# Kernel optimization log

Hardware: AMD Instinct MI355X
Metric: run time of the kernel (lower is better)

The kernel has to match this reference:

```python
import jax, jax.numpy as jnp
import numpy as np

SDF_W = 7000.0
EIK_W = 600.0
ORI_W = 500.0
NEAR_ORI_W = 10.0
GRADN_W = 200.0
K_NEIGHBORS = 2


def _orientation_sign(query, surface, normals, k=K_NEIGHBORS):
    # Original detaches to numpy for a scipy KDTree query -> stop_gradient here.
    q = jax.lax.stop_gradient(query)       # [Q,3]
    s = jax.lax.stop_gradient(surface)     # [S,3]
    n = jax.lax.stop_gradient(normals)     # [S,3]
    # Brute-force squared distances [Q,S] (GEMM-dominated).
    d2 = (jnp.sum(q * q, axis=-1, keepdims=True)
          - 2.0 * (q @ s.T)
          + jnp.sum(s * s, axis=-1)[None, :])
    _, idx = jax.lax.top_k(-d2, k)         # [Q,k] nearest-neighbor indices
    near_pts = s[idx]                      # [Q,k,3]
    near_nrm = n[idx]                      # [Q,k,3]
    vecs = q[:, None, :] - near_pts        # [Q,k,3]
    dots = jnp.sum(vecs * near_nrm, axis=-1)  # [Q,k]
    return jnp.sign(jnp.mean(dots, axis=1))   # [Q]


def setup_inputs() -> dict:
    key = jax.random.key(0)
    ks = jax.random.split(key, 8)
    N = 16384
    return {
        "manifold_pred": jax.random.normal(ks[0], (N, 1), jnp.float32) * 0.1,
        "manifold_grad": jax.random.normal(ks[1], (N, 3), jnp.float32),
        "nonmanifold_pred": jax.random.normal(ks[2], (N, 1), jnp.float32),
        "near_points_pred": jax.random.normal(ks[3], (N, 1), jnp.float32) * 0.1,
        "surface_points": jax.random.normal(ks[4], (N, 3), jnp.float32),
        "surface_normals": jax.random.normal(ks[5], (N, 3), jnp.float32),
        "off_surface_points": jax.random.normal(ks[6], (N, 3), jnp.float32) * 1.5,
        "near_points": jax.random.normal(ks[7], (N, 3), jnp.float32),
    }


def reference(manifold_pred, manifold_grad, nonmanifold_pred, near_points_pred,
              surface_points, surface_normals, off_surface_points, near_points):
    sdf_loss = jnp.mean(manifold_pred ** 2)
    eikonal_loss = jnp.mean((jnp.linalg.norm(manifold_grad, axis=-1) - 1.0) ** 2)

    signs_off = _orientation_sign(off_surface_points, surface_points, surface_normals)
    orientation_loss = jnp.mean(jax.nn.relu(-nonmanifold_pred * signs_off[:, None]))

    signs_near = _orientation_sign(near_points, surface_points, surface_normals)
    near_surface_orientation_loss = jnp.mean(jax.nn.relu(-near_points_pred * signs_near[:, None]))

    gradient_normal_loss = jnp.mean((manifold_grad - surface_normals) ** 2)

    total = (SDF_W * sdf_loss + EIK_W * eikonal_loss + ORI_W * orientation_loss
             + NEAR_ORI_W * near_surface_orientation_loss + GRADN_W * gradient_normal_loss)
    return (total, sdf_loss, eikonal_loss, orientation_loss,
            near_surface_orientation_loss, gradient_normal_loss)
```

## Files before the change

kernel.cpp:

```cpp
#include <hip/hip_runtime.h>
#include <math.h>

#define SDF_W      7000.0f
#define EIK_W      600.0f
#define ORI_W      500.0f
#define NEAR_ORI_W 10.0f
#define GRADN_W    200.0f

#define NWAVE  8
#define QW     16
#define CHKI   32
#define QPW    8


__device__ __forceinline__ float neg_half_norm2(float sx, float sy, float sz) {
    return -0.5f * fmaf(sx, sx, fmaf(sy, sy, sz * sz));
}
__device__ __forceinline__ float score(float qx, float qy, float qz,
                                       float sx, float sy, float sz, float nh) {
    return fmaf(qx, sx, fmaf(qy, sy, fmaf(qz, sz, nh)));
}

__device__ __forceinline__ float dot_fmt(const float4* __restrict__ fmt,
                                         const float* __restrict__ norms, int j,
                                         float qx, float qy, float qz) {
    float4 s = fmt[j];
    return fmaf(qx - s.x, norms[3*j],
           fmaf(qy - s.y, norms[3*j+1], (qz - s.z) * norms[3*j+2]));
}

__global__ __launch_bounds__(256) void fmt_k(
    const float* __restrict__ surf, float4* __restrict__ fmt, int S, int SPfull)
{
    int p = blockIdx.x * 256 + threadIdx.x;
    if (p >= SPfull) return;
    if (p < S) {
        float sx = surf[3*p], sy = surf[3*p+1], sz = surf[3*p+2];
        fmt[p] = make_float4(sx, sy, sz, neg_half_norm2(sx, sy, sz));
    } else {
        fmt[p] = make_float4(0.f, 0.f, 0.f, -3.0e38f);
    }
}

__global__ __launch_bounds__(512) __attribute__((amdgpu_waves_per_eu(2, 2)))
void nn_scan(const float* __restrict__ offq, const float* __restrict__ nearq,
             const float4* __restrict__ fmt, float4* __restrict__ recs,
             int nIter, int Qoff, int QT)
{
    const int lane = threadIdx.x & 63;
    const int wv   = __builtin_amdgcn_readfirstlane((int)threadIdx.x >> 6);
    const int qbase = (blockIdx.x * NWAVE + wv) * QW;

    float qx[QW], qy[QW], qz[QW];
    #pragma unroll
    for (int j = 0; j < QW; ++j) {
        int q = qbase + j;
        float x = 0.f, y = 0.f, z = 0.f;
        if (q < QT) {
            const float* p = (q < Qoff) ? (offq + 3 * q) : (nearq + 3 * (q - Qoff));
            x = p[0]; y = p[1]; z = p[2];
        }
        qx[j] = x; qy[j] = y; qz[j] = z;
    }

    float M1[QW], M2[QW];
    int id1[QW], id2[QW];
    #pragma unroll
    for (int j = 0; j < QW; ++j) {
        M1[j] = -3.0e38f; M2[j] = -3.0e38f; id1[j] = 0; id2[j] = 0;
    }

    const int nCh = (nIter + CHKI - 1) / CHKI;
    const float4* fp = fmt + lane;
    float4 cur = fp[0];
    int i = 0;
    #pragma unroll 1
    for (int cc = 0; cc < nCh; ++cc) {
        float P1[QW], P2[QW];
        #pragma unroll
        for (int j = 0; j < QW; ++j) { P1[j] = M1[j]; P2[j] = M2[j]; }
        const int iEnd = min(nIter, (cc + 1) * CHKI);
        #pragma unroll 2
        for (; i < iEnd; ++i) {
            float4 nxt = fp[(i + 1) * 64];
            #pragma unroll
            for (int j = 0; j < QW; ++j) {
                float g = score(qx[j], qy[j], qz[j], cur.x, cur.y, cur.z, cur.w);
                M2[j] = __builtin_amdgcn_fmed3f(g, M1[j], M2[j]);
                M1[j] = fmaxf(M1[j], g);
            }
            cur = nxt;
        }
        const int cid = (cc << 6) | lane;
        #pragma unroll
        for (int j = 0; j < QW; ++j) {
            id1[j] = (M1[j] != P1[j]) ? cid : id1[j];
            id2[j] = (M2[j] != P2[j]) ? cid : id2[j];
        }
    }

    #pragma unroll 1
    for (int j = 0; j < QW; ++j) {
        float m1 = M1[j], m2 = M2[j];
        int i1 = id1[j], i2 = id2[j];
        #pragma unroll
        for (int off = 32; off > 0; off >>= 1) {
            float b1 = __shfl_down(m1, off);
            float b2 = __shfl_down(m2, off);
            int   c1 = __shfl_down(i1, off);
            int   c2 = __shfl_down(i2, off);
            if (b1 > m1) {
                bool ka = (m1 > b2);
                m2 = ka ? m1 : b2;  i2 = ka ? i1 : c2;
                m1 = b1;            i1 = c1;
            } else {
                bool kb = (b1 > m2);
                m2 = kb ? b1 : m2;  i2 = kb ? c1 : i2;
            }
        }
        if (lane == 0 && qbase + j < QT)
            recs[qbase + j] = make_float4(m1, m2, __int_as_float(i1), __int_as_float(i2));
    }
}

__global__ __launch_bounds__(512) __attribute__((amdgpu_waves_per_eu(4, 4)))
void recover_k(const float* __restrict__ offq, const float* __restrict__ nearq,
               const float4* __restrict__ fmt, const float* __restrict__ norms,
               const float* __restrict__ nmpred, const float* __restrict__ nppred,
               const float* __restrict__ mp, const float* __restrict__ mg,
               const float* __restrict__ sn,
               const float4* __restrict__ recs, float* __restrict__ partials,
               int S, int Qoff, int QT, int N, int RB)
{
    const int t    = threadIdx.x;
    const int lane = t & 63;
    const int wv   = t >> 6;
    const int q0   = (blockIdx.x * NWAVE + wv) * QPW;

    float accOri = 0.f, accNori = 0.f;
    for (int u = 0; u < QPW; ++u) {
        int q = q0 + u;
        if (q >= QT) break;
        float4 r = recs[q];
        float M1 = r.x, M2 = r.y;
        int i1 = __float_as_int(r.z), i2 = __float_as_int(r.w);
        int cc1 = i1 >> 6, ln1 = i1 & 63;
        int cc2 = i2 >> 6, ln2 = i2 & 63;

        bool isNear = (q >= Qoff);
        const float* qp = isNear ? (nearq + 3 * (q - Qoff)) : (offq + 3 * q);
        float qx = qp[0], qy = qp[1], qz = qp[2];

        int half = lane >> 5;
        int k    = lane & 31;
        int p    = ((half ? cc2 : cc1) * CHKI + k) * 64 + (half ? ln2 : ln1);
        float target = half ? M2 : M1;
        float g = -3.0e38f, dotv = 0.f;
        if (p < S) {
            float4 s4 = fmt[p];
            g = score(qx, qy, qz, s4.x, s4.y, s4.z, s4.w);
            float nx = norms[3*p], ny = norms[3*p+1], nz = norms[3*p+2];
            dotv = fmaf(qx - s4.x, nx, fmaf(qy - s4.y, ny, (qz - s4.z) * nz));
        }
        unsigned long long m = __ballot(g == target);
        unsigned int lo = (unsigned int)m;
        unsigned int hi = (unsigned int)(m >> 32);

        float d1, d2;
        int k1 = -1;
        if (lo) {
            k1 = __ffs(lo) - 1;
            d1 = __shfl(dotv, k1);
        } else {
            d1 = dot_fmt(fmt, norms, 0, qx, qy, qz);
        }
        if (M1 == M2 && i1 == i2 && k1 >= 0) hi &= ~(1u << k1);
        if (hi) {
            int k2 = __ffs(hi) - 1;
            d2 = __shfl(dotv, 32 + k2);
        } else {
            int I1 = (k1 >= 0) ? ((cc1 * CHKI + k1) * 64 + ln1) : 0;
            int I2 = (I1 == 0 && S > 1) ? 1 : 0;
            d2 = dot_fmt(fmt, norms, I2, qx, qy, qz);
        }

        float ms = d1 + d2;
        float sgn = (ms > 0.f) ? 1.f : ((ms < 0.f) ? -1.f : 0.f);
        float pred = isNear ? nppred[q - Qoff] : nmpred[q];
        float term = fmaxf(0.f, -pred * sgn);
        if (lane == 0) {
            if (isNear) accNori += term; else accOri += term;
        }
    }

    float sdf = 0.f, eik = 0.f, gn = 0.f;
    for (int i = blockIdx.x * 512 + t; i < N; i += (int)gridDim.x * 512) {
        float p = mp[i];
        sdf += p * p;
        float gx = mg[3*i], gy = mg[3*i+1], gz = mg[3*i+2];
        float nrm = sqrtf(fmaf(gx, gx, fmaf(gy, gy, gz * gz)));
        float d = nrm - 1.0f;
        eik += d * d;
        float nx = sn[3*i], ny = sn[3*i+1], nz = sn[3*i+2];
        float dx = gx - nx, dy = gy - ny, dz = gz - nz;
        gn += fmaf(dx, dx, fmaf(dy, dy, dz * dz));
    }

    float v0 = accOri, v1 = accNori, v2 = sdf, v3 = eik, v4 = gn;
    #pragma unroll
    for (int off = 32; off > 0; off >>= 1) {
        v0 += __shfl_down(v0, off);
        v1 += __shfl_down(v1, off);
        v2 += __shfl_down(v2, off);
        v3 += __shfl_down(v3, off);
        v4 += __shfl_down(v4, off);
    }
    __shared__ float red[5][NWAVE];
    if (lane == 0) {
        red[0][wv] = v0; red[1][wv] = v1; red[2][wv] = v2;
        red[3][wv] = v3; red[4][wv] = v4;
    }
    __syncthreads();
    if (t == 0) {
        #pragma unroll
        for (int kk = 0; kk < 5; ++kk) {
            float s = 0.f;
            #pragma unroll
            for (int w = 0; w < NWAVE; ++w) s += red[kk][w];
            partials[kk * RB + blockIdx.x] = s;
        }
    }
}

__global__ __launch_bounds__(256) void final_k(
    const float* __restrict__ partials, float* __restrict__ out,
    int N, int RB, int Qoff, int Qnear)
{
    __shared__ float r[5][256];
    int t = threadIdx.x;
    float s[5] = {0.f, 0.f, 0.f, 0.f, 0.f};
    for (int i = t; i < RB; i += 256) {
        #pragma unroll
        for (int k = 0; k < 5; ++k) s[k] += partials[k * RB + i];
    }
    #pragma unroll
    for (int k = 0; k < 5; ++k) r[k][t] = s[k];
    __syncthreads();
    for (int off = 128; off > 0; off >>= 1) {
        if (t < off) {
            #pragma unroll
            for (int k = 0; k < 5; ++k) r[k][t] += r[k][t + off];
        }
        __syncthreads();
    }
    if (t == 0) {
        float orim  = r[0][0] / (float)Qoff;
        float norim = r[1][0] / (float)Qnear;
        float sdfm  = r[2][0] / (float)N;
        float eikm  = r[3][0] / (float)N;
        float gnm   = r[4][0] / (3.0f * (float)N);
        out[0] = SDF_W * sdfm + EIK_W * eikm + ORI_W * orim
               + NEAR_ORI_W * norim + GRADN_W * gnm;
        out[1] = sdfm;
        out[2] = eikm;
        out[3] = orim;
        out[4] = norim;
        out[5] = gnm;
    }
}

extern "C" void kernel_launch(void* const* d_in, const int* in_sizes, int n_in,
                              void* d_out, int out_size, void* d_ws, size_t ws_size,
                              hipStream_t stream)
{
    const float* mp    = (const float*)d_in[0];
    const float* mg    = (const float*)d_in[1];
    const float* nmp   = (const float*)d_in[2];
    const float* npp   = (const float*)d_in[3];
    const float* sp    = (const float*)d_in[4];
    const float* sn    = (const float*)d_in[5];
    const float* offp  = (const float*)d_in[6];
    const float* nearp = (const float*)d_in[7];
    float* out = (float*)d_out;

    const int N     = in_sizes[0];
    const int S     = in_sizes[4] / 3;
    const int Qoff  = in_sizes[2];
    const int Qnear = in_sizes[3];
    const int QT    = Qoff + Qnear;

    const int nIter  = (S + 63) / 64;
    const int SPfull = nIter * 64 + 64;

    float4* fmt      = (float4*)d_ws;
    float4* recs     = fmt + SPfull;
    float*  partials = (float*)(recs + QT);

    const int RB         = (QT + NWAVE * QPW - 1) / (NWAVE * QPW);
    const int scanBlocks = (QT + NWAVE * QW - 1) / (NWAVE * QW);

    fmt_k<<<(SPfull + 255) / 256, 256, 0, stream>>>(sp, fmt, S, SPfull);
    nn_scan<<<scanBlocks, 512, 0, stream>>>(offp, nearp, fmt, recs, nIter, Qoff, QT);
    recover_k<<<RB, 512, 0, stream>>>(offp, nearp, fmt, sn, nmp, npp,
                                      mp, mg, sn, recs, partials,
                                      S, Qoff, QT, N, RB);
    final_k<<<1, 256, 0, stream>>>(partials, out, N, RB, Qoff, Qnear);
}
```

Measured before the change: 179.0 us.

## Split the nearest-neighbor surface scan across two blocks and merge top-2 in recovery

The brute-force nearest-neighbor scan now divides the surface-point range into two chunk-aligned halves, each handled by a separate block. Each half writes its own top-2 record per query, and the recovery kernel merges the two partial top-2 lists before re-scoring. This doubles the number of scan blocks, which is meant to fill the GPU more fully and shorten the serial per-wave loop. The cost is an extra record write and merge per query, and the recovery kernel's occupancy hint is changed as well.

```diff
diff --git a/kernel.cpp b/kernel.cpp
--- a/kernel.cpp
+++ b/kernel.cpp
@@ -10,6 +10,7 @@
 #define NWAVE  8
 #define QW     16
 #define CHKI   32
+#define NSPLIT 2
 #define QPW    8
 
 
@@ -42,14 +43,19 @@
     }
 }
 
-__global__ __launch_bounds__(512) __attribute__((amdgpu_waves_per_eu(2, 2)))
+__global__ __launch_bounds__(512) __attribute__((amdgpu_waves_per_eu(2, 4)))
 void nn_scan(const float* __restrict__ offq, const float* __restrict__ nearq,
              const float4* __restrict__ fmt, float4* __restrict__ recs,
-             int nIter, int Qoff, int QT)
+             int nIter, int iPart, int Qoff, int QT)
 {
     const int lane = threadIdx.x & 63;
     const int wv   = __builtin_amdgcn_readfirstlane((int)threadIdx.x >> 6);
-    const int qbase = (blockIdx.x * NWAVE + wv) * QW;
+    const int part = blockIdx.x & (NSPLIT - 1);
+    const int qbase = ((blockIdx.x >> 1) * NWAVE + wv) * QW;
+
+    int iBeg = part * iPart;        if (iBeg > nIter) iBeg = nIter;
+    int iEndAll = iBeg + iPart;     if (iEndAll > nIter) iEndAll = nIter;
+    const int chunkBase = iBeg / CHKI;
 
     float qx[QW], qy[QW], qz[QW];
     #pragma unroll
@@ -70,16 +76,16 @@
         M1[j] = -3.0e38f; M2[j] = -3.0e38f; id1[j] = 0; id2[j] = 0;
     }
 
-    const int nCh = (nIter + CHKI - 1) / CHKI;
+    const int nCh = (iEndAll - iBeg + CHKI - 1) / CHKI;
     const float4* fp = fmt + lane;
-    float4 cur = fp[0];
-    int i = 0;
+    float4 cur = fp[iBeg * 64];
+    int i = iBeg;
     #pragma unroll 1
     for (int cc = 0; cc < nCh; ++cc) {
         float P1[QW], P2[QW];
         #pragma unroll
         for (int j = 0; j < QW; ++j) { P1[j] = M1[j]; P2[j] = M2[j]; }
-        const int iEnd = min(nIter, (cc + 1) * CHKI);
+        const int iEnd = min(iEndAll, iBeg + (cc + 1) * CHKI);
         #pragma unroll 2
         for (; i < iEnd; ++i) {
             float4 nxt = fp[(i + 1) * 64];
@@ -91,7 +97,7 @@
             }
             cur = nxt;
         }
-        const int cid = (cc << 6) | lane;
+        const int cid = ((chunkBase + cc) << 6) | lane;
         #pragma unroll
         for (int j = 0; j < QW; ++j) {
             id1[j] = (M1[j] != P1[j]) ? cid : id1[j];
@@ -119,11 +125,12 @@
             }
         }
         if (lane == 0 && qbase + j < QT)
-            recs[qbase + j] = make_float4(m1, m2, __int_as_float(i1), __int_as_float(i2));
-    }
-}
-
-__global__ __launch_bounds__(512) __attribute__((amdgpu_waves_per_eu(4, 4)))
+            recs[(qbase + j) * NSPLIT + part] =
+                make_float4(m1, m2, __int_as_float(i1), __int_as_float(i2));
+    }
+}
+
+__global__ __launch_bounds__(512) __attribute__((amdgpu_waves_per_eu(2, 2)))
 void recover_k(const float* __restrict__ offq, const float* __restrict__ nearq,
                const float4* __restrict__ fmt, const float* __restrict__ norms,
                const float* __restrict__ nmpred, const float* __restrict__ nppred,
@@ -141,9 +148,18 @@
     for (int u = 0; u < QPW; ++u) {
         int q = q0 + u;
         if (q >= QT) break;
-        float4 r = recs[q];
-        float M1 = r.x, M2 = r.y;
-        int i1 = __float_as_int(r.z), i2 = __float_as_int(r.w);
+
+        float M1 = -3.0e38f, M2 = -3.0e38f;
+        int i1 = 0, i2 = 0;
+        #pragma unroll
+        for (int h = 0; h < NSPLIT; ++h) {
+            float4 r = recs[q * NSPLIT + h];
+            float a1 = r.x, a2 = r.y;
+            int ac1 = __float_as_int(r.z), ac2 = __float_as_int(r.w);
+            if (a1 > M1)      { M2 = M1; i2 = i1; M1 = a1; i1 = ac1; }
+            else if (a1 > M2) { M2 = a1; i2 = ac1; }
+            if (a2 > M2)      { M2 = a2; i2 = ac2; }
+        }
         int cc1 = i1 >> 6, ln1 = i1 & 63;
         int cc2 = i2 >> 6, ln2 = i2 & 63;
 
@@ -291,16 +307,18 @@
 
     const int nIter  = (S + 63) / 64;
     const int SPfull = nIter * 64 + 64;
+    const int iPart  = (((nIter + NSPLIT - 1) / NSPLIT) + CHKI - 1) & ~(CHKI - 1);
 
     float4* fmt      = (float4*)d_ws;
     float4* recs     = fmt + SPfull;
-    float*  partials = (float*)(recs + QT);
+    float*  partials = (float*)(recs + (size_t)QT * NSPLIT);
 
     const int RB         = (QT + NWAVE * QPW - 1) / (NWAVE * QPW);
-    const int scanBlocks = (QT + NWAVE * QW - 1) / (NWAVE * QW);
+    const int scanBlocks = ((QT + NWAVE * QW - 1) / (NWAVE * QW)) * NSPLIT;
 
     fmt_k<<<(SPfull + 255) / 256, 256, 0, stream>>>(sp, fmt, S, SPfull);
-    nn_scan<<<scanBlocks, 512, 0, stream>>>(offp, nearp, fmt, recs, nIter, Qoff, QT);
+    nn_scan<<<scanBlocks, 512, 0, stream>>>(offp, nearp, fmt, recs,
+                                            nIter, iPart, Qoff, QT);
     recover_k<<<RB, 512, 0, stream>>>(offp, nearp, fmt, sn, nmp, npp,
                                       mp, mg, sn, recs, partials,
                                       S, Qoff, QT, N, RB);
```

After: 174.0 us. 1.03x faster.
